# Optimization experiments

Measured on AMD Instinct MI355X. Metric: run time of the kernel, lower is better.

Reference implementation:

```python
import jax, jax.numpy as jnp
import numpy as np

B, CIN, COUT, H, W = 64, 96, 96, 56, 56
MID = 192            # in_channels * expansion
SE_GROUPS = 12       # _nearest_divisor(192, 12)
SE_RED = 24          # ceil(max(192//8,4)/12)*12
EPS = 1e-5


def _apply_bn(x, p):
    # p: [4, C] = (gamma, beta, running_mean, running_var); eval-mode BN
    scale = p[0] * jax.lax.rsqrt(p[3] + EPS)
    shift = p[1] - p[2] * scale
    return x * scale[None, :, None, None] + shift[None, :, None, None]


def _shift_groups(x):
    h, w = x.shape[2], x.shape[3]
    x0, x1, x2, x3 = jnp.split(x, 4, axis=1)
    up = jnp.pad(x0, ((0, 0), (0, 0), (1, 0), (0, 0)))[:, :, :h, :]
    left = jnp.pad(x1, ((0, 0), (0, 0), (0, 0), (1, 0)))[:, :, :, :w]
    down = jnp.pad(x2, ((0, 0), (0, 0), (0, 1), (0, 0)))[:, :, 1:, :]
    right = jnp.pad(x3, ((0, 0), (0, 0), (0, 0), (0, 1)))[:, :, :, 1:]
    return jnp.concatenate([up, left, down, right], axis=1)


def _channel_shuffle(x, groups=4):
    b, c, h, w = x.shape
    x = x.reshape(b, groups, c // groups, h, w)
    x = jnp.transpose(x, (0, 2, 1, 3, 4))
    return x.reshape(b, c, h, w)


def _grouped_1x1(v, w, b, groups):
    # v: [B, Cin]; w: [Cout, Cin//groups, 1, 1]
    bsz = v.shape[0]
    cout = w.shape[0]
    vg = v.reshape(bsz, groups, -1)
    wg = w[:, :, 0, 0].reshape(groups, cout // groups, -1)
    out = jnp.einsum('bgi,goi->bgo', vg, wg).reshape(bsz, cout)
    return out + b


def _forward(x, expand_w, expand_bn, dw_w, dw_bn, id_w, id_bn, merge_bn,
             se_red_w, se_red_b, se_exp_w, se_exp_b, proj_w, proj_bn):
    # 1x1 expansion + BN + SiLU
    out = jnp.einsum('bchw,oc->bohw', x, expand_w[:, :, 0, 0])
    out = jax.nn.silu(_apply_bn(out, expand_bn))
    # shift-mix + channel shuffle (zero-FLOP data movement)
    out = _channel_shuffle(_shift_groups(out), groups=4)
    # depthwise 3x3 branch + BN
    dw = jax.lax.conv_general_dilated(
        out, dw_w, window_strides=(1, 1), padding=((1, 1), (1, 1)),
        feature_group_count=MID, dimension_numbers=('NCHW', 'OIHW', 'NCHW'))
    dw = _apply_bn(dw, dw_bn)
    # identity depthwise 1x1 branch (per-channel scale) + BN
    idb = _apply_bn(out * id_w[:, 0, 0, 0][None, :, None, None], id_bn)
    out = jax.nn.silu(_apply_bn(dw + idb, merge_bn))
    # grouped SE gating
    se = jnp.mean(out, axis=(2, 3))                     # [B, MID]
    se = jax.nn.relu(_grouped_1x1(se, se_red_w, se_red_b, SE_GROUPS))
    se = jax.nn.sigmoid(_grouped_1x1(se, se_exp_w, se_exp_b, SE_GROUPS))
    out = out * se[:, :, None, None]
    # 1x1 project + BN + residual + activation
    out = jnp.einsum('bchw,oc->bohw', out, proj_w[:, :, 0, 0])
    out = _apply_bn(out, proj_bn)
    out = out + x  # use_residual: stride==1 and in==out
    return jax.nn.silu(out)


def setup_inputs() -> dict:
    key = jax.random.key(0)
    ks = jax.random.split(key, 16)

    def bn_params(k, c):
        k1, k2, k3, k4 = jax.random.split(k, 4)
        gamma = 1.0 + 0.1 * jax.random.normal(k1, (c,), jnp.float32)
        beta = 0.1 * jax.random.normal(k2, (c,), jnp.float32)
        mean = 0.1 * jax.random.normal(k3, (c,), jnp.float32)
        var = 0.5 + jax.random.uniform(k4, (c,), jnp.float32)
        return jnp.stack([gamma, beta, mean, var])

    return {
        'x': jax.random.normal(ks[0], (B, CIN, H, W), jnp.float32),
        'expand_w': 0.1 * jax.random.normal(ks[1], (MID, CIN, 1, 1), jnp.float32),
        'expand_bn': bn_params(ks[2], MID),
        'dw_w': 0.2 * jax.random.normal(ks[3], (MID, 1, 3, 3), jnp.float32),
        'dw_bn': bn_params(ks[4], MID),
        'id_w': 0.2 * jax.random.normal(ks[5], (MID, 1, 1, 1), jnp.float32),
        'id_bn': bn_params(ks[6], MID),
        'merge_bn': bn_params(ks[7], MID),
        'se_red_w': 0.2 * jax.random.normal(ks[8], (SE_RED, MID // SE_GROUPS, 1, 1), jnp.float32),
        'se_red_b': 0.05 * jax.random.normal(ks[9], (SE_RED,), jnp.float32),
        'se_exp_w': 0.2 * jax.random.normal(ks[10], (MID, SE_RED // SE_GROUPS, 1, 1), jnp.float32),
        'se_exp_b': 0.05 * jax.random.normal(ks[11], (MID,), jnp.float32),
        'proj_w': 0.1 * jax.random.normal(ks[12], (COUT, MID, 1, 1), jnp.float32),
        'proj_bn': bn_params(ks[13], COUT),
    }


def reference(x, expand_w, expand_bn, dw_w, dw_bn, id_w, id_bn, merge_bn,
              se_red_w, se_red_b, se_exp_w, se_exp_b, proj_w, proj_bn):
    return _forward(x, expand_w, expand_bn, dw_w, dw_bn, id_w, id_bn, merge_bn,
                    se_red_w, se_red_b, se_exp_w, se_exp_b, proj_w, proj_bn)
```

## Files before the change

kernel.cpp:

```cpp
#include <hip/hip_runtime.h>
#include <hip/hip_bf16.h>

#define BB   64
#define CING 96
#define MIDC 192
#define HH   56
#define WWD  56
#define HWSZ (HH*WWD)
#define COUTC 96
#define BNEPS 1e-5f

typedef __attribute__((ext_vector_type(8))) short short8;
typedef __attribute__((ext_vector_type(8))) unsigned short ushort8v;
typedef __attribute__((ext_vector_type(4))) float float4v;
typedef unsigned short ushort_t;
typedef unsigned int uint_t;

__device__ __forceinline__ float siluf(float v){ return v / (1.f + __expf(-v)); }
__device__ __forceinline__ ushort_t f2bs(float f){
    uint_t u = __float_as_uint(f);
    uint_t r = u + 0x7FFFu + ((u >> 16) & 1u);
    return (ushort_t)(r >> 16);
}
__device__ __forceinline__ float bs2f(ushort_t u){
    return __uint_as_float(((uint_t)u) << 16);
}

__global__ __launch_bounds__(256) void k0_setup(
    const float* __restrict__ expand_w, const float* __restrict__ expand_bn,
    const float* __restrict__ dw_w, const float* __restrict__ dw_bn,
    const float* __restrict__ id_w, const float* __restrict__ id_bn,
    const float* __restrict__ merge_bn,
    const float* __restrict__ proj_w, const float* __restrict__ proj_bn,
    ushort_t* __restrict__ Aexp, float* __restrict__ ebias,
    float* __restrict__ w9f, float* __restrict__ cstf,
    ushort_t* __restrict__ Aproj, float* __restrict__ pscf, float* __restrict__ pshf)
{
    int i = blockIdx.x*256 + threadIdx.x;
    if (i < 4608) {
        int m = i/24, kq = (i%24)*4;
        int ic = (m&3)*48 + (m>>2);
        float sc0 = expand_bn[ic]*rsqrtf(expand_bn[3*MIDC+ic]+BNEPS);
        #pragma unroll
        for (int j=0;j<4;j++) Aexp[m*96+kq+j] = f2bs(expand_w[ic*96+kq+j]*sc0);
        if (kq==0) ebias[m] = expand_bn[MIDC+ic] - expand_bn[2*MIDC+ic]*sc0;
    } else if (i < 9216) {
        int ii = i-4608; int m = ii/48, kq = (ii%48)*4;
        #pragma unroll
        for (int j=0;j<4;j++) Aproj[m*MIDC+kq+j] = f2bs(proj_w[m*MIDC+kq+j]);
        if (kq==0){
            float sc = proj_bn[m]*rsqrtf(proj_bn[3*COUTC+m]+BNEPS);
            pscf[m]=sc; pshf[m]=proj_bn[COUTC+m]-proj_bn[2*COUTC+m]*sc;
        }
    } else if (i < 9408) {
        int oc = i-9216;
        float sc1 = dw_bn[oc]    * rsqrtf(dw_bn[3*MIDC+oc]    + BNEPS);
        float sh1 = dw_bn[MIDC+oc]    - dw_bn[2*MIDC+oc]*sc1;
        float sc2 = id_bn[oc]    * rsqrtf(id_bn[3*MIDC+oc]    + BNEPS);
        float sh2 = id_bn[MIDC+oc]    - id_bn[2*MIDC+oc]*sc2;
        float sc3 = merge_bn[oc] * rsqrtf(merge_bn[3*MIDC+oc] + BNEPS);
        float sh3 = merge_bn[MIDC+oc] - merge_bn[2*MIDC+oc]*sc3;
        float A = sc3*sc1;
        #pragma unroll
        for (int j=0;j<9;j++) w9f[oc*9+j] = A*dw_w[oc*9+j];
        w9f[oc*9+4] += sc3*sc2*id_w[oc];
        cstf[oc] = sc3*(sh1+sh2) + sh3;
    }
}

#define LDB1T 104
__global__ __launch_bounds__(256) void k1_expand(
    const float* __restrict__ x,
    const ushort_t* __restrict__ Aexp,
    const float* __restrict__ ebias,
    ushort_t* __restrict__ EY)
{
    __shared__ __align__(16) ushort_t BsT[64*LDB1T];
    __shared__ float ebL[MIDC];
    const int t = threadIdx.x;
    const int p0 = blockIdx.x*64, b = blockIdx.y;

    if (t < MIDC) ebL[t] = ebias[t];
    {
        const int n  = t & 63;
        const int kb = (t >> 6)*24;
        #pragma unroll
        for (int ii = 0; ii < 3; ii++) {
            int k8 = kb + ii*8;
            const float* xp = x + ((size_t)(b*CING + k8))*HWSZ + p0 + n;
            ushort8v u;
            #pragma unroll
            for (int j = 0; j < 8; j++) u[j] = f2bs(xp[(size_t)j*HWSZ]);
            *(ushort8v*)(&BsT[n*LDB1T + k8]) = u;
        }
    }

    const int lane = t & 63, wv = t >> 6;
    const int l = lane & 15, q = lane >> 4;
    short8 af[3][3];
    #pragma unroll
    for (int ks = 0; ks < 3; ks++)
        #pragma unroll
        for (int mi = 0; mi < 3; mi++)
            af[ks][mi] = *(const short8*)(Aexp + ((wv*3+mi)*16 + l)*96 + ks*32 + q*8);
    __syncthreads();

    float4v acc[3][4];
    #pragma unroll
    for (int mi=0;mi<3;mi++)
        #pragma unroll
        for (int nt=0;nt<4;nt++) acc[mi][nt] = (float4v){0.f,0.f,0.f,0.f};
    #pragma unroll
    for (int ks = 0; ks < 3; ks++) {
        const int k0 = ks*32;
        short8 bf[4];
        #pragma unroll
        for (int nt = 0; nt < 4; nt++)
            bf[nt] = *(const short8*)(&BsT[(nt*16 + l)*LDB1T + k0 + q*8]);
        #pragma unroll
        for (int mi = 0; mi < 3; mi++)
            #pragma unroll
            for (int nt = 0; nt < 4; nt++)
                acc[mi][nt] = __builtin_amdgcn_mfma_f32_16x16x32_bf16(af[ks][mi], bf[nt], acc[mi][nt], 0,0,0);
    }
    #pragma unroll
    for (int mi = 0; mi < 3; mi++) {
        #pragma unroll
        for (int r = 0; r < 4; r++) {
            int m = (wv*3+mi)*16 + q*4 + r;
            float eb = ebL[m];
            size_t rowb = (size_t)(b*MIDC + m)*HWSZ + p0 + l;
            #pragma unroll
            for (int nt = 0; nt < 4; nt++)
                EY[rowb + nt*16] = f2bs(siluf(acc[mi][nt][r] + eb));
        }
    }
}

__global__ __launch_bounds__(256) void k2_dw(
    ushort_t* __restrict__ EY,
    const float* __restrict__ w9f,
    const float* __restrict__ cstf,
    float* __restrict__ sums)
{
    const int t = threadIdx.x;
    const int lane = t & 63, wv = t >> 6;
    const int oc = blockIdx.x*4 + wv;
    const int b  = blockIdx.y;
    ushort_t* plane = EY + (size_t)(b*MIDC + oc)*HWSZ;
    const int g  = oc & 3;
    const int dy = (g==0)?-1:(g==2?1:0);
    const int dx = (g==1)?-1:(g==3?1:0);
    float w9[9];
    #pragma unroll
    for (int j=0;j<9;j++) w9[j] = w9f[oc*9+j];
    const float cst = cstf[oc];

    const int c  = lane;
    const int cx = c + dx;
    const bool laneok = (c < WWD) & (cx >= 0) & (cx < WWD);
    const int cxc = min(max(cx, 0), WWD-1);
    const bool cval = (c < WWD);

    float p1 = 0.f, p0 = 0.f, partial = 0.f;
    for (int y = -1; y <= HH; y++) {
        int yy = y + dy;
        float val = 0.f;
        if (y >= 0 && y < HH && yy >= 0 && yy < HH) {
            float v = bs2f(plane[yy*WWD + cxc]);
            val = laneok ? v : 0.f;
        }
        float vl = __shfl_up(val, 1);  if (lane == 0) vl = 0.f;
        float vr = __shfl_down(val, 1);
        float a0 = w9[0]*vl + w9[1]*val + w9[2]*vr;
        float a1 = w9[3]*vl + w9[4]*val + w9[5]*vr;
        float a2 = w9[6]*vl + w9[7]*val + w9[8]*vr;
        if (y >= 1) {
            float yv = siluf(p1 + a2 + cst);
            if (cval) {
                plane[(y-1)*WWD + c] = f2bs(yv);
                partial += yv;
            }
        }
        p1 = p0 + a1;
        p0 = a0;
    }
    #pragma unroll
    for (int off=1; off<64; off<<=1) partial += __shfl_xor(partial, off);
    if (lane == 0) sums[b*MIDC + oc] = partial;
}

__global__ __launch_bounds__(192) void k3_se(
    const float* __restrict__ sums,
    const float* __restrict__ se_red_w, const float* __restrict__ se_red_b,
    const float* __restrict__ se_exp_w, const float* __restrict__ se_exp_b,
    float* __restrict__ sews)
{
    __shared__ float meanL[MIDC];
    __shared__ float redL[24];
    const int b = blockIdx.x, t = threadIdx.x;
    meanL[t] = sums[b*MIDC + t] * (1.f/(float)HWSZ);
    __syncthreads();
    if (t < 24) {
        int g = t >> 1;
        float a = se_red_b[t];
        #pragma unroll
        for (int i = 0; i < 16; i++) a += meanL[g*16+i] * se_red_w[t*16+i];
        redL[t] = fmaxf(a, 0.f);
    }
    __syncthreads();
    int g = t >> 4;
    float a = se_exp_b[t] + redL[g*2]*se_exp_w[t*2] + redL[g*2+1]*se_exp_w[t*2+1];
    sews[b*MIDC + t] = 1.f/(1.f + __expf(-a));
}

#define LDB4T 200
__global__ __launch_bounds__(256) void k4_proj(
    const ushort_t* __restrict__ EY,
    const float* __restrict__ sews,
    const ushort_t* __restrict__ Aproj,
    const float* __restrict__ pscf, const float* __restrict__ pshf,
    const float* __restrict__ x,
    float* __restrict__ out)
{
    __shared__ __align__(16) ushort_t BsT[64*LDB4T];
    __shared__ float pscL[COUTC], pshL[COUTC];
    const int t = threadIdx.x;
    const int p0 = blockIdx.x*64, b = blockIdx.y;
    if (t < COUTC) { pscL[t] = pscf[t]; pshL[t] = pshf[t]; }
    {
        const int n  = t & 63;
        const int kb = (t >> 6)*48;
        const float* sew = sews + b*MIDC;
        #pragma unroll
        for (int ii = 0; ii < 6; ii++) {
            int k8 = kb + ii*8;
            const ushort_t* ep = EY + ((size_t)(b*MIDC + k8))*HWSZ + p0 + n;
            ushort8v u;
            #pragma unroll
            for (int j = 0; j < 8; j++)
                u[j] = f2bs(bs2f(ep[(size_t)j*HWSZ]) * sew[k8+j]);
            *(ushort8v*)(&BsT[n*LDB4T + k8]) = u;
        }
    }

    const int lane = t & 63, wv = t >> 6;
    const int l = lane & 15, q = lane >> 4;
    const int mh = wv >> 1, nh = wv & 1;
    short8 af[6][3];
    #pragma unroll
    for (int ks = 0; ks < 6; ks++)
        #pragma unroll
        for (int mi = 0; mi < 3; mi++)
            af[ks][mi] = *(const short8*)(Aproj + ((mh*3+mi)*16 + l)*MIDC + ks*32 + q*8);
    __syncthreads();

    float4v acc[3][2];
    #pragma unroll
    for (int mi=0;mi<3;mi++)
        #pragma unroll
        for (int nt=0;nt<2;nt++) acc[mi][nt] = (float4v){0.f,0.f,0.f,0.f};
    #pragma unroll
    for (int ks = 0; ks < 6; ks++) {
        const int k0 = ks*32;
        short8 bf[2];
        #pragma unroll
        for (int nt = 0; nt < 2; nt++)
            bf[nt] = *(const short8*)(&BsT[(nh*32 + nt*16 + l)*LDB4T + k0 + q*8]);
        #pragma unroll
        for (int mi = 0; mi < 3; mi++)
            #pragma unroll
            for (int nt = 0; nt < 2; nt++)
                acc[mi][nt] = __builtin_amdgcn_mfma_f32_16x16x32_bf16(af[ks][mi], bf[nt], acc[mi][nt], 0,0,0);
    }
    #pragma unroll
    for (int mi = 0; mi < 3; mi++) {
        #pragma unroll
        for (int r = 0; r < 4; r++) {
            int m = (mh*3+mi)*16 + q*4 + r;
            float sc = pscL[m], sh = pshL[m];
            size_t rowb = (size_t)(b*COUTC + m)*HWSZ + p0 + nh*32 + l;
            #pragma unroll
            for (int nt = 0; nt < 2; nt++) {
                size_t idx = rowb + nt*16;
                out[idx] = siluf(acc[mi][nt][r]*sc + sh + x[idx]);
            }
        }
    }
}

extern "C" void kernel_launch(void* const* d_in, const int* in_sizes, int n_in,
                              void* d_out, int out_size, void* d_ws, size_t ws_size,
                              hipStream_t stream)
{
    const float* x         = (const float*)d_in[0];
    const float* expand_w  = (const float*)d_in[1];
    const float* expand_bn = (const float*)d_in[2];
    const float* dw_w      = (const float*)d_in[3];
    const float* dw_bn     = (const float*)d_in[4];
    const float* id_w      = (const float*)d_in[5];
    const float* id_bn     = (const float*)d_in[6];
    const float* merge_bn  = (const float*)d_in[7];
    const float* se_red_w  = (const float*)d_in[8];
    const float* se_red_b  = (const float*)d_in[9];
    const float* se_exp_w  = (const float*)d_in[10];
    const float* se_exp_b  = (const float*)d_in[11];
    const float* proj_w    = (const float*)d_in[12];
    const float* proj_bn   = (const float*)d_in[13];

    char* base = (char*)d_ws;
    size_t off = 0;
    ushort_t* EY   = (ushort_t*)(base + off); off += (size_t)BB*MIDC*HWSZ*2;
    float* sums    = (float*)(base + off);    off += BB*MIDC*4;
    float* sews    = (float*)(base + off);    off += BB*MIDC*4;
    ushort_t* Aexp = (ushort_t*)(base + off); off += MIDC*CING*2;
    ushort_t* Aproj= (ushort_t*)(base + off); off += COUTC*MIDC*2;
    float* ebias   = (float*)(base + off);    off += MIDC*4;
    float* w9f     = (float*)(base + off);    off += MIDC*9*4;
    float* cstf    = (float*)(base + off);    off += MIDC*4;
    float* pscf    = (float*)(base + off);    off += COUTC*4;
    float* pshf    = (float*)(base + off);    off += COUTC*4;

    k0_setup<<<dim3(37), dim3(256), 0, stream>>>(
        expand_w, expand_bn, dw_w, dw_bn, id_w, id_bn, merge_bn, proj_w, proj_bn,
        Aexp, ebias, w9f, cstf, Aproj, pscf, pshf);
    k1_expand<<<dim3(HWSZ/64, BB), dim3(256), 0, stream>>>(x, Aexp, ebias, EY);
    k2_dw<<<dim3(MIDC/4, BB), dim3(256), 0, stream>>>(EY, w9f, cstf, sums);
    k3_se<<<dim3(BB), dim3(192), 0, stream>>>(
        sums, se_red_w, se_red_b, se_exp_w, se_exp_b, sews);
    k4_proj<<<dim3(HWSZ/64, BB), dim3(256), 0, stream>>>(
        EY, sews, Aproj, pscf, pshf, x, (float*)d_out);
}
```

Before: 289.2 us.

## Vectorize MFMA epilogue stores and split depthwise planes across two waves

Swaps the MFMA operand order so each lane holds four consecutive pixels of a single output channel. This lets the expand and projection epilogues write packed bf16 pairs and float4 vectors instead of scattered scalar stores. The depthwise kernel now splits each channel plane into two row halves handled by separate waves, preloading the boundary rows before a barrier to avoid in-place read/write hazards, and combines the partial sums in shared memory. Conversion now uses packed bf16 intrinsics, and the depthwise launch doubles its grid for more parallelism, at the cost of the extra sync and boundary-handling logic.

```diff
diff --git a/kernel.cpp b/kernel.cpp
--- a/kernel.cpp
+++ b/kernel.cpp
@@ -24,6 +24,10 @@
 }
 __device__ __forceinline__ float bs2f(ushort_t u){
     return __uint_as_float(((uint_t)u) << 16);
+}
+__device__ __forceinline__ uint_t pkbf(float a, float b){
+    __hip_bfloat162 h = __float22bfloat162_rn(make_float2(a, b));
+    union { __hip_bfloat162 h; uint_t u; } cv; cv.h = h; return cv.u;
 }
 
 __global__ __launch_bounds__(256) void k0_setup(
@@ -88,10 +92,13 @@
         for (int ii = 0; ii < 3; ii++) {
             int k8 = kb + ii*8;
             const float* xp = x + ((size_t)(b*CING + k8))*HWSZ + p0 + n;
-            ushort8v u;
+            float v[8];
             #pragma unroll
-            for (int j = 0; j < 8; j++) u[j] = f2bs(xp[(size_t)j*HWSZ]);
-            *(ushort8v*)(&BsT[n*LDB1T + k8]) = u;
+            for (int j = 0; j < 8; j++) v[j] = xp[(size_t)j*HWSZ];
+            uint4 uu;
+            uu.x = pkbf(v[0],v[1]); uu.y = pkbf(v[2],v[3]);
+            uu.z = pkbf(v[4],v[5]); uu.w = pkbf(v[6],v[7]);
+            *(uint4*)(&BsT[n*LDB1T + k8]) = uu;
         }
     }
 
@@ -121,18 +128,21 @@
         for (int mi = 0; mi < 3; mi++)
             #pragma unroll
             for (int nt = 0; nt < 4; nt++)
-                acc[mi][nt] = __builtin_amdgcn_mfma_f32_16x16x32_bf16(af[ks][mi], bf[nt], acc[mi][nt], 0,0,0);
+                acc[mi][nt] = __builtin_amdgcn_mfma_f32_16x16x32_bf16(bf[nt], af[ks][mi], acc[mi][nt], 0,0,0);
     }
     #pragma unroll
     for (int mi = 0; mi < 3; mi++) {
-        #pragma unroll
-        for (int r = 0; r < 4; r++) {
-            int m = (wv*3+mi)*16 + q*4 + r;
-            float eb = ebL[m];
-            size_t rowb = (size_t)(b*MIDC + m)*HWSZ + p0 + l;
-            #pragma unroll
-            for (int nt = 0; nt < 4; nt++)
-                EY[rowb + nt*16] = f2bs(siluf(acc[mi][nt][r] + eb));
+        const int m = (wv*3+mi)*16 + l;
+        const float eb = ebL[m];
+        ushort_t* rp = EY + (size_t)(b*MIDC + m)*HWSZ + p0 + q*4;
+        #pragma unroll
+        for (int nt = 0; nt < 4; nt++) {
+            float s0 = siluf(acc[mi][nt][0] + eb);
+            float s1 = siluf(acc[mi][nt][1] + eb);
+            float s2 = siluf(acc[mi][nt][2] + eb);
+            float s3 = siluf(acc[mi][nt][3] + eb);
+            uint2 w2; w2.x = pkbf(s0,s1); w2.y = pkbf(s2,s3);
+            *(uint2*)(rp + nt*16) = w2;
         }
     }
 }
@@ -143,9 +153,11 @@
     const float* __restrict__ cstf,
     float* __restrict__ sums)
 {
+    __shared__ float wred[4];
     const int t = threadIdx.x;
-    const int lane = t & 63, wv = t >> 6;
-    const int oc = blockIdx.x*4 + wv;
+    const int lane = t & 63, w = t >> 6;
+    const int pl = w >> 1, half = w & 1;
+    const int oc = blockIdx.x*2 + pl;
     const int b  = blockIdx.y;
     ushort_t* plane = EY + (size_t)(b*MIDC + oc)*HWSZ;
     const int g  = oc & 3;
@@ -162,21 +174,40 @@
     const int cxc = min(max(cx, 0), WWD-1);
     const bool cval = (c < WWD);
 
+    int ya = -1000, yb = -1000;
+    if (half == 0) { if (dy == 1) { ya = 27; yb = 28; } else if (dy == 0) { ya = 28; } }
+    else           { if (dy == -1){ ya = 27; yb = 28; } else if (dy == 0) { ya = 27; } }
+    float va = 0.f, vb = 0.f;
+    if (ya != -1000) {
+        float v = bs2f(plane[(ya+dy)*WWD + cxc]);
+        va = laneok ? v : 0.f;
+    }
+    if (yb != -1000) {
+        float v = bs2f(plane[(yb+dy)*WWD + cxc]);
+        vb = laneok ? v : 0.f;
+    }
+    __syncthreads();
+
+    const int ys = half ? 27 : -1;
+    const int ye = half ? 56 : 28;
+    const int so = half ? 29 : 1;
     float p1 = 0.f, p0 = 0.f, partial = 0.f;
-    for (int y = -1; y <= HH; y++) {
+    for (int y = ys; y <= ye; ++y) {
         int yy = y + dy;
         float val = 0.f;
-        if (y >= 0 && y < HH && yy >= 0 && yy < HH) {
+        if (((unsigned)y < HH) & ((unsigned)yy < HH)) {
             float v = bs2f(plane[yy*WWD + cxc]);
             val = laneok ? v : 0.f;
         }
+        if (y == ya) val = va;
+        if (y == yb) val = vb;
         float vl = __shfl_up(val, 1);  if (lane == 0) vl = 0.f;
         float vr = __shfl_down(val, 1);
         float a0 = w9[0]*vl + w9[1]*val + w9[2]*vr;
         float a1 = w9[3]*vl + w9[4]*val + w9[5]*vr;
-        float a2 = w9[6]*vl + w9[7]*val + w9[8]*vr;
-        if (y >= 1) {
-            float yv = siluf(p1 + a2 + cst);
+        float a2 = w9[6]*vl + w9[7]*val + w9[8]*vr + cst;
+        if (y >= so) {
+            float yv = siluf(p1 + a2);
             if (cval) {
                 plane[(y-1)*WWD + c] = f2bs(yv);
                 partial += yv;
@@ -187,7 +218,9 @@
     }
     #pragma unroll
     for (int off=1; off<64; off<<=1) partial += __shfl_xor(partial, off);
-    if (lane == 0) sums[b*MIDC + oc] = partial;
+    if (lane == 0) wred[w] = partial;
+    __syncthreads();
+    if (t < 2) sums[b*MIDC + blockIdx.x*2 + t] = wred[t*2] + wred[t*2+1];
 }
 
 __global__ __launch_bounds__(192) void k3_se(
@@ -236,11 +269,14 @@
         for (int ii = 0; ii < 6; ii++) {
             int k8 = kb + ii*8;
             const ushort_t* ep = EY + ((size_t)(b*MIDC + k8))*HWSZ + p0 + n;
-            ushort8v u;
+            float v[8];
             #pragma unroll
             for (int j = 0; j < 8; j++)
-                u[j] = f2bs(bs2f(ep[(size_t)j*HWSZ]) * sew[k8+j]);
-            *(ushort8v*)(&BsT[n*LDB4T + k8]) = u;
+                v[j] = bs2f(ep[(size_t)j*HWSZ]) * sew[k8+j];
+            uint4 uu;
+            uu.x = pkbf(v[0],v[1]); uu.y = pkbf(v[2],v[3]);
+            uu.z = pkbf(v[4],v[5]); uu.w = pkbf(v[6],v[7]);
+            *(uint4*)(&BsT[n*LDB4T + k8]) = uu;
         }
     }
 
@@ -271,20 +307,23 @@
         for (int mi = 0; mi < 3; mi++)
             #pragma unroll
             for (int nt = 0; nt < 2; nt++)
-                acc[mi][nt] = __builtin_amdgcn_mfma_f32_16x16x32_bf16(af[ks][mi], bf[nt], acc[mi][nt], 0,0,0);
+                acc[mi][nt] = __builtin_amdgcn_mfma_f32_16x16x32_bf16(bf[nt], af[ks][mi], acc[mi][nt], 0,0,0);
     }
     #pragma unroll
     for (int mi = 0; mi < 3; mi++) {
-        #pragma unroll
-        for (int r = 0; r < 4; r++) {
-            int m = (mh*3+mi)*16 + q*4 + r;
-            float sc = pscL[m], sh = pshL[m];
-            size_t rowb = (size_t)(b*COUTC + m)*HWSZ + p0 + nh*32 + l;
-            #pragma unroll
-            for (int nt = 0; nt < 2; nt++) {
-                size_t idx = rowb + nt*16;
-                out[idx] = siluf(acc[mi][nt][r]*sc + sh + x[idx]);
-            }
+        const int m = (mh*3+mi)*16 + l;
+        const float sc = pscL[m], sh = pshL[m];
+        const size_t rowb = (size_t)(b*COUTC + m)*HWSZ + p0 + nh*32 + q*4;
+        #pragma unroll
+        for (int nt = 0; nt < 2; nt++) {
+            const size_t idx = rowb + nt*16;
+            float4 xr = *(const float4*)(x + idx);
+            float4 o;
+            o.x = siluf(acc[mi][nt][0]*sc + sh + xr.x);
+            o.y = siluf(acc[mi][nt][1]*sc + sh + xr.y);
+            o.z = siluf(acc[mi][nt][2]*sc + sh + xr.z);
+            o.w = siluf(acc[mi][nt][3]*sc + sh + xr.w);
+            *(float4*)(out + idx) = o;
         }
     }
 }
@@ -325,7 +364,7 @@
         expand_w, expand_bn, dw_w, dw_bn, id_w, id_bn, merge_bn, proj_w, proj_bn,
         Aexp, ebias, w9f, cstf, Aproj, pscf, pshf);
     k1_expand<<<dim3(HWSZ/64, BB), dim3(256), 0, stream>>>(x, Aexp, ebias, EY);
-    k2_dw<<<dim3(MIDC/4, BB), dim3(256), 0, stream>>>(EY, w9f, cstf, sums);
+    k2_dw<<<dim3(MIDC/2, BB), dim3(256), 0, stream>>>(EY, w9f, cstf, sums);
     k3_se<<<dim3(BB), dim3(192), 0, stream>>>(
         sums, se_red_w, se_red_b, se_exp_w, se_exp_b, sews);
     k4_proj<<<dim3(HWSZ/64, BB), dim3(256), 0, stream>>>(
```

Result: slower. 300.5 us (+3.9%).

## Vectorize depthwise kernel: 4 pixels per lane, split plane rows across waves

Applied to the files above, without the earlier changes.

The depthwise 3x3 kernel is restructured. Each lane now handles 4 adjacent columns through packed 64-bit bf16 loads and stores. Each wave covers 4 channels (16 lanes per plane), and two waves split the height in halves, saving the boundary rows before a barrier so the in-place update stays correct. Shift direction is templated, which removes the per-lane branches and the 8 idle lanes per 64 seen in the old one-column-per-lane layout. The costs are a block-wide sync, more register pressure, and halo bookkeeping that makes the code more complex.

```diff
diff --git a/kernel.cpp b/kernel.cpp
--- a/kernel.cpp
+++ b/kernel.cpp
@@ -25,6 +25,12 @@
 __device__ __forceinline__ float bs2f(ushort_t u){
     return __uint_as_float(((uint_t)u) << 16);
 }
+__device__ __forceinline__ uint_t pkbf(float a, float b){
+    __hip_bfloat162 h = __float22bfloat162_rn(make_float2(a, b));
+    union { __hip_bfloat162 h; uint_t u; } cv; cv.h = h; return cv.u;
+}
+__device__ __forceinline__ float bslo(uint_t x){ return __uint_as_float(x << 16); }
+__device__ __forceinline__ float bshi(uint_t x){ return __uint_as_float(x & 0xFFFF0000u); }
 
 __global__ __launch_bounds__(256) void k0_setup(
     const float* __restrict__ expand_w, const float* __restrict__ expand_bn,
@@ -137,57 +143,98 @@
     }
 }
 
-__global__ __launch_bounds__(256) void k2_dw(
+template<int DY, int DX>
+__device__ __forceinline__ float dw_plane(
+    ushort_t* __restrict__ plane, const float* __restrict__ w9, float cst,
+    int li, int h, bool act)
+{
+    uint2 pA = make_uint2(0u,0u), pB = make_uint2(0u,0u);
+    int rA = -100, rB = -100;
+    if (h == 0) { if (DY==1){ rA=28; rB=29; } else if (DY==0){ rA=28; } }
+    else        { if (DY==-1){ rA=26; rB=27; } else if (DY==0){ rA=27; } }
+    const ushort_t* pl = plane + li*4;
+    if (rA >= 0) pA = *(const uint2*)(pl + rA*WWD);
+    if (rB >= 0) pB = *(const uint2*)(pl + rB*WWD);
+    __syncthreads();
+
+    const int ys = h ? 27 : -1;
+    const int so = h ? 29 : 1;
+
+    auto loadrow = [&](int y) -> uint2 {
+        int yy = y + DY;
+        uint2 u = make_uint2(0u,0u);
+        if (((unsigned)y < (unsigned)HH) && ((unsigned)yy < (unsigned)HH)) {
+            if (yy == rA)      u = pA;
+            else if (yy == rB) u = pB;
+            else               u = *(const uint2*)(pl + yy*WWD);
+        }
+        return u;
+    };
+
+    float p0[4] = {0,0,0,0}, p1[4] = {0,0,0,0};
+    float partial = 0.f;
+    uint2 u = loadrow(ys);
+    for (int y = ys; y <= ys + 29; ++y) {
+        uint2 un = loadrow(y + 1);
+        uint_t lhi = __shfl_up(u.y, 1);
+        uint_t rlo = __shfl_down(u.x, 1);
+        if (li == 0)  lhi = 0u;
+        if (li == 13) rlo = 0u;
+        float s[8];
+        s[0]=bslo(lhi); s[1]=bshi(lhi);
+        s[2]=bslo(u.x); s[3]=bshi(u.x);
+        s[4]=bslo(u.y); s[5]=bshi(u.y);
+        s[6]=bslo(rlo); s[7]=bshi(rlo);
+        if (li == 0)  s[DX+1] = 0.f;
+        if (li == 13) s[DX+6] = 0.f;
+        float o[4];
+        #pragma unroll
+        for (int j = 0; j < 4; j++) {
+            float t0 = s[j+DX+1], t1 = s[j+DX+2], t2 = s[j+DX+3];
+            o[j]  = p1[j] + (w9[6]*t0 + w9[7]*t1 + w9[8]*t2) + cst;
+            p1[j] = p0[j] + (w9[3]*t0 + w9[4]*t1 + w9[5]*t2);
+            p0[j] =          w9[0]*t0 + w9[1]*t1 + w9[2]*t2;
+        }
+        if (y >= so && act) {
+            float y0=siluf(o[0]), y1=siluf(o[1]), y2=siluf(o[2]), y3=siluf(o[3]);
+            uint2 w2; w2.x = pkbf(y0,y1); w2.y = pkbf(y2,y3);
+            *(uint2*)(plane + (size_t)(y-1)*WWD + li*4) = w2;
+            partial += (y0+y1) + (y2+y3);
+        }
+        u = un;
+    }
+    #pragma unroll
+    for (int off = 1; off < 16; off <<= 1) partial += __shfl_xor(partial, off);
+    return partial;
+}
+
+__global__ __launch_bounds__(128) void k2_dw(
     ushort_t* __restrict__ EY,
     const float* __restrict__ w9f,
     const float* __restrict__ cstf,
     float* __restrict__ sums)
 {
+    __shared__ float wred[8];
     const int t = threadIdx.x;
-    const int lane = t & 63, wv = t >> 6;
-    const int oc = blockIdx.x*4 + wv;
-    const int b  = blockIdx.y;
+    const int lane = t & 63, h = t >> 6;
+    const int lg = lane >> 4, li = lane & 15;
+    const int gi = blockIdx.x >> 2, r = blockIdx.x & 3;
+    const int b = blockIdx.y;
+    const int oc = gi*16 + r + lg*4;
     ushort_t* plane = EY + (size_t)(b*MIDC + oc)*HWSZ;
-    const int g  = oc & 3;
-    const int dy = (g==0)?-1:(g==2?1:0);
-    const int dx = (g==1)?-1:(g==3?1:0);
     float w9[9];
     #pragma unroll
-    for (int j=0;j<9;j++) w9[j] = w9f[oc*9+j];
+    for (int j = 0; j < 9; j++) w9[j] = w9f[oc*9+j];
     const float cst = cstf[oc];
-
-    const int c  = lane;
-    const int cx = c + dx;
-    const bool laneok = (c < WWD) & (cx >= 0) & (cx < WWD);
-    const int cxc = min(max(cx, 0), WWD-1);
-    const bool cval = (c < WWD);
-
-    float p1 = 0.f, p0 = 0.f, partial = 0.f;
-    for (int y = -1; y <= HH; y++) {
-        int yy = y + dy;
-        float val = 0.f;
-        if (y >= 0 && y < HH && yy >= 0 && yy < HH) {
-            float v = bs2f(plane[yy*WWD + cxc]);
-            val = laneok ? v : 0.f;
-        }
-        float vl = __shfl_up(val, 1);  if (lane == 0) vl = 0.f;
-        float vr = __shfl_down(val, 1);
-        float a0 = w9[0]*vl + w9[1]*val + w9[2]*vr;
-        float a1 = w9[3]*vl + w9[4]*val + w9[5]*vr;
-        float a2 = w9[6]*vl + w9[7]*val + w9[8]*vr;
-        if (y >= 1) {
-            float yv = siluf(p1 + a2 + cst);
-            if (cval) {
-                plane[(y-1)*WWD + c] = f2bs(yv);
-                partial += yv;
-            }
-        }
-        p1 = p0 + a1;
-        p0 = a0;
-    }
-    #pragma unroll
-    for (int off=1; off<64; off<<=1) partial += __shfl_xor(partial, off);
-    if (lane == 0) sums[b*MIDC + oc] = partial;
+    const bool act = (li < 14);
+    float ps;
+    if      (r == 0) ps = dw_plane<-1, 0>(plane, w9, cst, li, h, act);
+    else if (r == 1) ps = dw_plane< 0,-1>(plane, w9, cst, li, h, act);
+    else if (r == 2) ps = dw_plane< 1, 0>(plane, w9, cst, li, h, act);
+    else             ps = dw_plane< 0, 1>(plane, w9, cst, li, h, act);
+    if (li == 0) wred[h*4 + lg] = ps;
+    __syncthreads();
+    if (t < 4) sums[b*MIDC + gi*16 + r + t*4] = wred[t] + wred[4 + t];
 }
 
 __global__ __launch_bounds__(192) void k3_se(
@@ -283,7 +330,8 @@
             #pragma unroll
             for (int nt = 0; nt < 2; nt++) {
                 size_t idx = rowb + nt*16;
-                out[idx] = siluf(acc[mi][nt][r]*sc + sh + x[idx]);
+                float v = acc[mi][nt][r]*sc + sh + x[idx];
+                out[idx] = siluf(v);
             }
         }
     }
@@ -325,7 +373,7 @@
         expand_w, expand_bn, dw_w, dw_bn, id_w, id_bn, merge_bn, proj_w, proj_bn,
         Aexp, ebias, w9f, cstf, Aproj, pscf, pshf);
     k1_expand<<<dim3(HWSZ/64, BB), dim3(256), 0, stream>>>(x, Aexp, ebias, EY);
-    k2_dw<<<dim3(MIDC/4, BB), dim3(256), 0, stream>>>(EY, w9f, cstf, sums);
+    k2_dw<<<dim3(48, BB), dim3(128), 0, stream>>>(EY, w9f, cstf, sums);
     k3_se<<<dim3(BB), dim3(192), 0, stream>>>(
         sums, se_red_w, se_red_b, se_exp_w, se_exp_b, sews);
     k4_proj<<<dim3(HWSZ/64, BB), dim3(256), 0, stream>>>(
```

Result: faster. 279.5 us (-3.4%).
